# Performance work log

Measured on AMD Instinct MI355X. Metric: run time of the kernel, lower is better.

The kernel has to match this reference:

```python
import jax, jax.numpy as jnp
import numpy as np

B, D_MODEL, N, H = 4, 256, 2048, 4
HEAD_DIM = D_MODEL // H  # 64


def _rotate_half(x):
    # x: [..., d] with d even; pairs (x1, x2) -> (-x2, x1)
    x = x.reshape(x.shape[:-1] + (x.shape[-1] // 2, 2))
    x1, x2 = x[..., 0], x[..., 1]
    return jnp.stack((-x2, x1), axis=-1).reshape(x.shape[:-2] + (-1,))


def _apply_rope(freqs, t):
    # freqs: [2, n, d] (cos, sin); t: [b, h, n, d]
    return t * freqs[0] + _rotate_half(t) * freqs[1]


def setup_inputs() -> dict:
    key = jax.random.key(0)
    ks = jax.random.split(key, 12)
    s = 0.02
    inp = {
        "query": jax.random.normal(ks[0], (B, D_MODEL, N), jnp.float32),
        "key": jax.random.normal(ks[1], (B, D_MODEL, N), jnp.float32),
        "value": jax.random.normal(ks[2], (B, D_MODEL, N), jnp.float32),
        "encoding": jax.random.normal(ks[3], (2, N, HEAD_DIM), jnp.float32),
        "Wq": jax.random.normal(ks[4], (D_MODEL, D_MODEL), jnp.float32) * s,
        "bq": jnp.zeros((D_MODEL,), jnp.float32),
        "Wk": jax.random.normal(ks[5], (D_MODEL, D_MODEL), jnp.float32) * s,
        "bk": jnp.zeros((D_MODEL,), jnp.float32),
        "Wv": jax.random.normal(ks[6], (D_MODEL, D_MODEL), jnp.float32) * s,
        "bv": jnp.zeros((D_MODEL,), jnp.float32),
        "Wm": jax.random.normal(ks[7], (D_MODEL, D_MODEL), jnp.float32) * s,
        "bm": jnp.zeros((D_MODEL,), jnp.float32),
    }
    return inp


def _proj(W, b, x):
    # 1x1 Conv1d == channel matmul: x [b, c_in, n] -> [b, c_out, n]
    return jnp.einsum('oi,bin->bon', W, x) + b[None, :, None]


def reference(query, key, value, encoding, Wq, bq, Wk, bk, Wv, bv, Wm, bm):
    b = query.shape[0]
    # project and split channels into (head_dim, heads): [b, d, h, n]
    q = _proj(Wq, bq, query).reshape(b, HEAD_DIM, H, -1)
    k = _proj(Wk, bk, key).reshape(b, HEAD_DIM, H, -1)
    v = _proj(Wv, bv, value).reshape(b, HEAD_DIM, H, -1)
    # RoPE on [b, h, n, d] layout
    q = jnp.transpose(_apply_rope(encoding, jnp.transpose(q, (0, 2, 3, 1))), (0, 3, 1, 2))
    k = jnp.transpose(_apply_rope(encoding, jnp.transpose(k, (0, 2, 3, 1))), (0, 3, 1, 2))
    # attention: scores [b, h, n, m]
    scores = jnp.einsum('bdhn,bdhm->bhnm', q, k) / jnp.sqrt(jnp.float32(HEAD_DIM))
    prob = jax.nn.softmax(scores, axis=-1)
    x = jnp.einsum('bhnm,bdhm->bdhn', prob, v)
    x = x.reshape(b, HEAD_DIM * H, -1)
    return _proj(Wm, bm, x)
```

## Files before the change

kernel.cpp:

```cpp
#include <hip/hip_runtime.h>
#include <stdint.h>

#define NSEQ 2048

typedef __attribute__((ext_vector_type(4))) float f32x4;
typedef __attribute__((ext_vector_type(8))) short s16x8;
typedef _Float16 f16x8 __attribute__((ext_vector_type(8)));

#define OFF_XT  0u
#define OFF_PO  0u
#define OFF_M   16777216u
#define OFF_L   17301504u
#define OFF_QR  17825792u
#define OFF_KR  22020096u
#define OFF_VT  26214400u

__device__ __forceinline__ short f2h(float f) {
  _Float16 h = (_Float16)f;
  return __builtin_bit_cast(short, h);
}
__device__ __forceinline__ float h2f(short s) {
  return (float)__builtin_bit_cast(_Float16, s);
}
__device__ __forceinline__ int swz128(int row, int slot) {
  return row * 128 + ((slot ^ (row & 7)) << 4);
}
#define MFMA(a, b, c) __builtin_amdgcn_mfma_f32_16x16x32_f16(a, b, c, 0, 0, 0)

__global__ __launch_bounds__(256) void k_trans(const float* __restrict__ q,
    const float* __restrict__ k, const float* __restrict__ v, char* __restrict__ ws) {
  int tensor = blockIdx.z >> 2, b = blockIdx.z & 3;
  const float* src = tensor == 0 ? q : (tensor == 1 ? k : v);
  short* dst = (short*)(ws + OFF_XT) + (tensor * 4 + b) * 524288;
  int n0 = blockIdx.x * 64, i0 = blockIdx.y * 64;
  __shared__ float tile[64][65];
  int t = threadIdx.x;
  int nl = t & 63, ib = (t >> 6) * 16;
#pragma unroll
  for (int r = 0; r < 16; ++r)
    tile[ib + r][nl] = src[(b * 256 + i0 + ib + r) * 2048 + n0 + nl];
  __syncthreads();
  int nr = t >> 2, ic = (t & 3) * 16;
  short tmp[16];
#pragma unroll
  for (int j = 0; j < 16; ++j) tmp[j] = f2h(tile[ic + j][nr]);
  short* dp = &dst[(n0 + nr) * 256 + i0 + ic];
  *(s16x8*)dp = *(const s16x8*)&tmp[0];
  *(s16x8*)(dp + 8) = *(const s16x8*)&tmp[8];
}

__global__ __launch_bounds__(256) void k_proj(const float* __restrict__ Wq,
    const float* __restrict__ Wk, const float* __restrict__ Wv,
    const float* __restrict__ enc, const float* __restrict__ bq,
    const float* __restrict__ bk, const float* __restrict__ bv, char* __restrict__ ws) {
  int proj = blockIdx.z >> 2, b = blockIdx.z & 3;
  const float* W = proj == 0 ? Wq : (proj == 1 ? Wk : Wv);
  const short* X = (const short*)(ws + OFF_XT) + (proj * 4 + b) * 524288;
  int o0 = blockIdx.y * 64, n0 = blockIdx.x * 64;
  __shared__ short As[64 * 64], Bs[64 * 64];
  int t = threadIdx.x, lane = t & 63, g = lane >> 4, c = lane & 15, wave = t >> 6;
  int wr = wave >> 1, wc = wave & 1;
  int row = t >> 2, seg = t & 3;
  f32x4 acc[2][2] = {};
  for (int kk = 0; kk < 4; ++kk) {
    __syncthreads();
    int koff = kk * 64;
    const float* wsrc = &W[(o0 + row) * 256 + koff + seg * 16];
    short ha[16];
#pragma unroll
    for (int q4 = 0; q4 < 4; ++q4) {
      f32x4 wv4 = *(const f32x4*)(wsrc + q4 * 4);
#pragma unroll
      for (int j = 0; j < 4; ++j) ha[q4 * 4 + j] = f2h(wv4[j]);
    }
    *(s16x8*)((char*)As + swz128(row, seg * 2))     = *(const s16x8*)&ha[0];
    *(s16x8*)((char*)As + swz128(row, seg * 2 + 1)) = *(const s16x8*)&ha[8];
    const short* xsrc = &X[(n0 + row) * 256 + koff];
    *(s16x8*)((char*)Bs + swz128(row, seg))     = *(const s16x8*)(xsrc + seg * 8);
    *(s16x8*)((char*)Bs + swz128(row, 4 + seg)) = *(const s16x8*)(xsrc + 32 + seg * 8);
    __syncthreads();
#pragma unroll
    for (int ks = 0; ks < 2; ++ks) {
      f16x8 af[2], bfr[2];
#pragma unroll
      for (int f = 0; f < 2; ++f) {
        af[f]  = *(const f16x8*)((char*)As + swz128(wr * 32 + f * 16 + c, ks * 4 + g));
        bfr[f] = *(const f16x8*)((char*)Bs + swz128(wc * 32 + f * 16 + c, ks * 4 + g));
      }
#pragma unroll
      for (int i = 0; i < 2; ++i)
#pragma unroll
        for (int j = 0; j < 2; ++j)
          acc[i][j] = MFMA(af[i], bfr[j], acc[i][j]);
    }
  }
  const float* bias = proj == 0 ? bq : (proj == 1 ? bk : bv);
  if (proj < 2) {
    short* dst0 = (short*)(ws + (proj == 0 ? OFF_QR : OFF_KR));
    float scale = proj == 0 ? 0.18033688f : 1.0f;
    float sgn = (g & 1) ? 1.0f : -1.0f;
#pragma unroll
    for (int i = 0; i < 2; ++i) {
      int ob = o0 + wr * 32 + i * 16 + g * 4;
      int d = ob >> 2;
#pragma unroll
      for (int j = 0; j < 2; ++j) {
        int n = n0 + wc * 32 + j * 16 + c;
        float cv = enc[n * 64 + d], sv = enc[131072 + n * 64 + d];
#pragma unroll
        for (int r = 0; r < 4; ++r) {
          float val = acc[i][j][r] + bias[ob + r];
          float par = __shfl_xor(val, 16, 64);
          float res = (val * cv + sgn * par * sv) * scale;
          dst0[((b * 4 + r) * 2048 + n) * 64 + d] = f2h(res);
        }
      }
    }
  } else {
    short* dst = (short*)(ws + OFF_VT);
#pragma unroll
    for (int i = 0; i < 2; ++i) {
      int ob = o0 + wr * 32 + i * 16 + g * 4;
      int d = ob >> 2;
#pragma unroll
      for (int j = 0; j < 2; ++j) {
        int n = n0 + wc * 32 + j * 16 + c;
#pragma unroll
        for (int r = 0; r < 4; ++r) {
          float val = acc[i][j][r] + bias[ob + r];
          dst[((b * 4 + r) * 64 + d) * 2048 + n] = f2h(val);
        }
      }
    }
  }
}

__global__ __launch_bounds__(256, 4) void k_attn(char* __restrict__ ws) {
  int bh = blockIdx.y, ms = blockIdx.z;
  int t = threadIdx.x, wave = t >> 6, lane = t & 63, g = lane >> 4, c = lane & 15;
  int nw = blockIdx.x * 64 + wave * 16;
  const short* Q = (const short*)(ws + OFF_QR) + bh * 131072;
  const short* K = (const short*)(ws + OFF_KR) + bh * 131072;
  const short* V = (const short*)(ws + OFF_VT) + bh * 131072;
  __shared__ short Ks[64 * 64], Vs[64 * 64], Ps[4][16 * 64];
  char* Pb = (char*)Ps[wave];
  f16x8 qf0 = *(const f16x8*)&Q[(nw + c) * 64 + g * 8];
  f16x8 qf1 = *(const f16x8*)&Q[(nw + c) * 64 + 32 + g * 8];
  f32x4 po[4] = {};
  float mrun = -1e30f, lrun = 0.f;
  int sr = t >> 3, sl = t & 7;
  const int mb = ms * 512;
  int bsrc = g * 16 + g * 4;

  s16x8 RA[4], RB[4];
  auto LD = [&](int m0, s16x8* R) {
    R[0] = *(const s16x8*)&K[(m0 + sr) * 64 + sl * 8];
    R[1] = *(const s16x8*)&K[(m0 + sr + 32) * 64 + sl * 8];
    R[2] = *(const s16x8*)&V[sr * 2048 + m0 + sl * 8];
    R[3] = *(const s16x8*)&V[(sr + 32) * 2048 + m0 + sl * 8];
  };
  auto ST = [&](const s16x8* R) {
    *(s16x8*)((char*)Ks + swz128(sr, sl))      = R[0];
    *(s16x8*)((char*)Ks + swz128(sr + 32, sl)) = R[1];
    *(s16x8*)((char*)Vs + swz128(sr, sl))      = R[2];
    *(s16x8*)((char*)Vs + swz128(sr + 32, sl)) = R[3];
  };
  auto COMPUTE = [&]() {
    f32x4 s[4] = {};
    __builtin_amdgcn_s_setprio(1);
#pragma unroll
    for (int fj = 0; fj < 4; ++fj) {
      f16x8 k0 = *(const f16x8*)((char*)Ks + swz128(fj * 16 + c, g));
      f16x8 k1 = *(const f16x8*)((char*)Ks + swz128(fj * 16 + c, 4 + g));
      s[fj] = MFMA(k0, qf0, s[fj]);
      s[fj] = MFMA(k1, qf1, s[fj]);
    }
    __builtin_amdgcn_s_setprio(0);
    float t0 = fmaxf(fmaxf(s[0][0], s[0][1]), fmaxf(s[0][2], s[0][3]));
    float t1 = fmaxf(fmaxf(s[1][0], s[1][1]), fmaxf(s[1][2], s[1][3]));
    float t2 = fmaxf(fmaxf(s[2][0], s[2][1]), fmaxf(s[2][2], s[2][3]));
    float t3 = fmaxf(fmaxf(s[3][0], s[3][1]), fmaxf(s[3][2], s[3][3]));
    float rmax = fmaxf(fmaxf(t0, t1), fmaxf(t2, t3));
    rmax = fmaxf(rmax, __shfl_xor(rmax, 16, 64));
    rmax = fmaxf(rmax, __shfl_xor(rmax, 32, 64));
    if (__any(rmax > mrun + 11.5f)) {
      float nm = fmaxf(mrun, rmax);
      float corr = exp2f(mrun - nm);
      mrun = nm;
      lrun *= corr;
#pragma unroll
      for (int r = 0; r < 4; ++r) {
        float corr_r = __shfl(corr, bsrc + r, 64);
#pragma unroll
        for (int fd = 0; fd < 4; ++fd) po[fd][r] *= corr_r;
      }
    }
    float p[4][4], rs = 0.f;
#pragma unroll
    for (int fj = 0; fj < 4; ++fj) {
      f32x4 pv;
#pragma unroll
      for (int r = 0; r < 4; ++r) {
        pv[r] = exp2f(s[fj][r] - mrun);
        p[fj][r] = pv[r];
      }
      rs += (pv[0] + pv[1]) + (pv[2] + pv[3]);
    }
    rs += __shfl_xor(rs, 16, 64);
    rs += __shfl_xor(rs, 32, 64);
    lrun += rs;
#pragma unroll
    for (int fj = 0; fj < 4; ++fj)
#pragma unroll
      for (int r = 0; r < 4; ++r) {
        int mm = fj * 16 + g * 4 + r;
        *(short*)(Pb + swz128(c, mm >> 3) + (mm & 7) * 2) = f2h(p[fj][r]);
      }
    asm volatile("s_waitcnt lgkmcnt(0)" ::: "memory");
    __builtin_amdgcn_sched_barrier(0);
    f16x8 pa0 = *(const f16x8*)(Pb + swz128(c, g));
    f16x8 pa1 = *(const f16x8*)(Pb + swz128(c, 4 + g));
    __builtin_amdgcn_s_setprio(1);
#pragma unroll
    for (int fd = 0; fd < 4; ++fd) {
      int dd = fd * 16 + c;
      f16x8 vb0 = *(const f16x8*)((char*)Vs + swz128(dd, g));
      f16x8 vb1 = *(const f16x8*)((char*)Vs + swz128(dd, 4 + g));
      po[fd] = MFMA(pa0, vb0, po[fd]);
      po[fd] = MFMA(pa1, vb1, po[fd]);
    }
    __builtin_amdgcn_s_setprio(0);
  };

  LD(mb, RA);
  for (int tt = 0; tt < 8; tt += 2) {
    __syncthreads();
    ST(RA);
    LD(mb + (tt + 1) * 64, RB);
    __syncthreads();
    COMPUTE();
    __syncthreads();
    ST(RB);
    if (tt + 2 < 8) LD(mb + (tt + 2) * 64, RA);
    __syncthreads();
    COMPUTE();
  }

  short* PO = (short*)(ws + OFF_PO);
  float* Mm = (float*)(ws + OFF_M);
  float* Ll = (float*)(ws + OFF_L);
  int base = (ms * 16 + bh) * 2048;
  float li[4];
#pragma unroll
  for (int r = 0; r < 4; ++r) li[r] = 1.0f / __shfl(lrun, bsrc + r, 64);
#pragma unroll
  for (int fd = 0; fd < 4; ++fd) {
    int d = fd * 16 + c;
#pragma unroll
    for (int r = 0; r < 4; ++r) {
      int n = nw + g * 4 + r;
      PO[(base + n) * 64 + d] = f2h(po[fd][r] * li[r]);
    }
  }
  if (g == 0) {
    Mm[base + nw + c] = mrun;
    Ll[base + nw + c] = lrun;
  }
}

__global__ __launch_bounds__(256) void k_final(const float* __restrict__ Wm,
    const float* __restrict__ bm, float* __restrict__ out, char* __restrict__ ws) {
  int b = blockIdx.z;
  int o0 = blockIdx.y * 64, n0 = blockIdx.x * 64;
  const short* PO = (const short*)(ws + OFF_PO);
  const float* Mm = (const float*)(ws + OFF_M);
  const float* Ll = (const float*)(ws + OFF_L);
  __shared__ short As[64 * 64], Bs[64 * 64];
  int t = threadIdx.x, lane = t & 63, g = lane >> 4, c = lane & 15, wave = t >> 6;
  int wr = wave >> 1, wc = wave & 1;
  int row = t >> 2, seg = t & 3;
  f32x4 acc[2][2] = {};
  for (int kk = 0; kk < 4; ++kk) {
    __syncthreads();
    short ha[16];
#pragma unroll
    for (int j = 0; j < 16; ++j)
      ha[j] = f2h(Wm[(o0 + row) * 256 + (seg * 16 + j) * 4 + kk]);
    *(s16x8*)((char*)As + swz128(row, seg * 2))     = *(const s16x8*)&ha[0];
    *(s16x8*)((char*)As + swz128(row, seg * 2 + 1)) = *(const s16x8*)&ha[8];
    int bh = b * 4 + kk;
    int nr = n0 + row;
    float m0 = Mm[(0 * 16 + bh) * 2048 + nr], l0 = Ll[(0 * 16 + bh) * 2048 + nr];
    float m1 = Mm[(1 * 16 + bh) * 2048 + nr], l1 = Ll[(1 * 16 + bh) * 2048 + nr];
    float m2 = Mm[(2 * 16 + bh) * 2048 + nr], l2 = Ll[(2 * 16 + bh) * 2048 + nr];
    float m3 = Mm[(3 * 16 + bh) * 2048 + nr], l3 = Ll[(3 * 16 + bh) * 2048 + nr];
    float M = fmaxf(fmaxf(m0, m1), fmaxf(m2, m3));
    float w0 = l0 * exp2f(m0 - M), w1 = l1 * exp2f(m1 - M);
    float w2 = l2 * exp2f(m2 - M), w3 = l3 * exp2f(m3 - M);
    float inv = 1.f / (w0 + w1 + w2 + w3);
    w0 *= inv; w1 *= inv; w2 *= inv; w3 *= inv;
    float cb[16];
    {
      const short* p0 = &PO[((0 * 16 + bh) * 2048 + nr) * 64 + seg * 16];
      const short* p1 = &PO[((1 * 16 + bh) * 2048 + nr) * 64 + seg * 16];
      const short* p2 = &PO[((2 * 16 + bh) * 2048 + nr) * 64 + seg * 16];
      const short* p3 = &PO[((3 * 16 + bh) * 2048 + nr) * 64 + seg * 16];
      s16x8 a0 = *(const s16x8*)p0, a1 = *(const s16x8*)(p0 + 8);
      s16x8 b0 = *(const s16x8*)p1, b1 = *(const s16x8*)(p1 + 8);
      s16x8 c0 = *(const s16x8*)p2, c1 = *(const s16x8*)(p2 + 8);
      s16x8 d0 = *(const s16x8*)p3, d1 = *(const s16x8*)(p3 + 8);
#pragma unroll
      for (int j = 0; j < 8; ++j) {
        cb[j]     = w0 * h2f(a0[j]) + w1 * h2f(b0[j]) + w2 * h2f(c0[j]) + w3 * h2f(d0[j]);
        cb[j + 8] = w0 * h2f(a1[j]) + w1 * h2f(b1[j]) + w2 * h2f(c1[j]) + w3 * h2f(d1[j]);
      }
    }
    short hb[16];
#pragma unroll
    for (int j = 0; j < 16; ++j) hb[j] = f2h(cb[j]);
    *(s16x8*)((char*)Bs + swz128(row, seg * 2))     = *(const s16x8*)&hb[0];
    *(s16x8*)((char*)Bs + swz128(row, seg * 2 + 1)) = *(const s16x8*)&hb[8];
    __syncthreads();
#pragma unroll
    for (int ks = 0; ks < 2; ++ks) {
      f16x8 af[2], bfr[2];
#pragma unroll
      for (int f = 0; f < 2; ++f) {
        af[f]  = *(const f16x8*)((char*)As + swz128(wr * 32 + f * 16 + c, ks * 4 + g));
        bfr[f] = *(const f16x8*)((char*)Bs + swz128(wc * 32 + f * 16 + c, ks * 4 + g));
      }
#pragma unroll
      for (int i = 0; i < 2; ++i)
#pragma unroll
        for (int j = 0; j < 2; ++j)
          acc[i][j] = MFMA(af[i], bfr[j], acc[i][j]);
    }
  }
#pragma unroll
  for (int i = 0; i < 2; ++i) {
    int ob = o0 + wr * 32 + i * 16 + g * 4;
#pragma unroll
    for (int j = 0; j < 2; ++j) {
      int n = n0 + wc * 32 + j * 16 + c;
#pragma unroll
      for (int r = 0; r < 4; ++r)
        out[(b * 256 + ob + r) * 2048 + n] = acc[i][j][r] + bm[ob + r];
    }
  }
}

extern "C" void kernel_launch(void* const* d_in, const int* in_sizes, int n_in,
                              void* d_out, int out_size, void* d_ws, size_t ws_size,
                              hipStream_t stream) {
  (void)in_sizes; (void)n_in; (void)out_size; (void)ws_size;
  const float* q   = (const float*)d_in[0];
  const float* k   = (const float*)d_in[1];
  const float* v   = (const float*)d_in[2];
  const float* enc = (const float*)d_in[3];
  const float* Wq  = (const float*)d_in[4];
  const float* bq  = (const float*)d_in[5];
  const float* Wk  = (const float*)d_in[6];
  const float* bk  = (const float*)d_in[7];
  const float* Wv  = (const float*)d_in[8];
  const float* bv  = (const float*)d_in[9];
  const float* Wm  = (const float*)d_in[10];
  const float* bm  = (const float*)d_in[11];
  char* ws = (char*)d_ws;
  float* out = (float*)d_out;
  hipLaunchKernelGGL(k_trans, dim3(32, 4, 12), dim3(256), 0, stream, q, k, v, ws);
  hipLaunchKernelGGL(k_proj, dim3(32, 4, 12), dim3(256), 0, stream, Wq, Wk, Wv, enc, bq, bk, bv, ws);
  hipLaunchKernelGGL(k_attn, dim3(32, 16, 4), dim3(256), 0, stream, ws);
  hipLaunchKernelGGL(k_final, dim3(32, 4, 4), dim3(256), 0, stream, Wm, bm, out, ws);
}
```

Measured before the change: 161.1 us.

## Process two query tiles per wave in attention and remap blocks across XCDs

Each attention wave now handles 32 query rows (two 16-row MFMA tiles) instead of 16. Each K/V tile loaded into shared memory is reused for twice the work, and the attention grid is halved. Block indices in k_proj, k_attn and k_final are remapped so that neighbouring logical tiles land on the same XCD (blocks are assumed round-robin over 8 XCDs), which should improve L2 locality. The cost is more registers per thread for the doubled accumulators and softmax state, which may reduce occupancy under the 4-blocks-per-CU launch bound.

```diff
diff --git a/kernel.cpp b/kernel.cpp
--- a/kernel.cpp
+++ b/kernel.cpp
@@ -53,10 +53,13 @@
     const float* __restrict__ Wk, const float* __restrict__ Wv,
     const float* __restrict__ enc, const float* __restrict__ bq,
     const float* __restrict__ bk, const float* __restrict__ bv, char* __restrict__ ws) {
-  int proj = blockIdx.z >> 2, b = blockIdx.z & 3;
+  int hid = blockIdx.x + 32 * (blockIdx.y + 4 * blockIdx.z);
+  int fm = (hid & 7) * 192 + (hid >> 3);
+  int yo = fm & 3, xn = (fm >> 2) & 31, z = fm >> 7;
+  int proj = z >> 2, b = z & 3;
   const float* W = proj == 0 ? Wq : (proj == 1 ? Wk : Wv);
   const short* X = (const short*)(ws + OFF_XT) + (proj * 4 + b) * 524288;
-  int o0 = blockIdx.y * 64, n0 = blockIdx.x * 64;
+  int o0 = yo * 64, n0 = xn * 64;
   __shared__ short As[64 * 64], Bs[64 * 64];
   int t = threadIdx.x, lane = t & 63, g = lane >> 4, c = lane & 15, wave = t >> 6;
   int wr = wave >> 1, wc = wave & 1;
@@ -136,18 +139,22 @@
 }
 
 __global__ __launch_bounds__(256, 4) void k_attn(char* __restrict__ ws) {
-  int bh = blockIdx.y, ms = blockIdx.z;
+  int hid = blockIdx.x + 16 * (blockIdx.y + 16 * blockIdx.z);
+  int fm = (hid & 7) * 128 + (hid >> 3);
+  int qx = fm & 15, bh = (fm >> 4) & 15, ms = fm >> 8;
   int t = threadIdx.x, wave = t >> 6, lane = t & 63, g = lane >> 4, c = lane & 15;
-  int nw = blockIdx.x * 64 + wave * 16;
+  int nw = qx * 128 + wave * 32;
   const short* Q = (const short*)(ws + OFF_QR) + bh * 131072;
   const short* K = (const short*)(ws + OFF_KR) + bh * 131072;
   const short* V = (const short*)(ws + OFF_VT) + bh * 131072;
-  __shared__ short Ks[64 * 64], Vs[64 * 64], Ps[4][16 * 64];
+  __shared__ short Ks[64 * 64], Vs[64 * 64], Ps[4][32 * 64];
   char* Pb = (char*)Ps[wave];
-  f16x8 qf0 = *(const f16x8*)&Q[(nw + c) * 64 + g * 8];
-  f16x8 qf1 = *(const f16x8*)&Q[(nw + c) * 64 + 32 + g * 8];
-  f32x4 po[4] = {};
-  float mrun = -1e30f, lrun = 0.f;
+  f16x8 qa0 = *(const f16x8*)&Q[(nw + c) * 64 + g * 8];
+  f16x8 qa1 = *(const f16x8*)&Q[(nw + c) * 64 + 32 + g * 8];
+  f16x8 qb0 = *(const f16x8*)&Q[(nw + 16 + c) * 64 + g * 8];
+  f16x8 qb1 = *(const f16x8*)&Q[(nw + 16 + c) * 64 + 32 + g * 8];
+  f32x4 poA[4] = {}, poB[4] = {};
+  float mrA = -1e30f, lrA = 0.f, mrB = -1e30f, lrB = 0.f;
   int sr = t >> 3, sl = t & 7;
   const int mb = ms * 512;
   int bsrc = g * 16 + g * 4;
@@ -166,68 +173,93 @@
     *(s16x8*)((char*)Vs + swz128(sr + 32, sl)) = R[3];
   };
   auto COMPUTE = [&]() {
-    f32x4 s[4] = {};
+    f32x4 sA[4] = {}, sB[4] = {};
     __builtin_amdgcn_s_setprio(1);
 #pragma unroll
     for (int fj = 0; fj < 4; ++fj) {
       f16x8 k0 = *(const f16x8*)((char*)Ks + swz128(fj * 16 + c, g));
       f16x8 k1 = *(const f16x8*)((char*)Ks + swz128(fj * 16 + c, 4 + g));
-      s[fj] = MFMA(k0, qf0, s[fj]);
-      s[fj] = MFMA(k1, qf1, s[fj]);
+      sA[fj] = MFMA(k0, qa0, sA[fj]);
+      sB[fj] = MFMA(k0, qb0, sB[fj]);
+      sA[fj] = MFMA(k1, qa1, sA[fj]);
+      sB[fj] = MFMA(k1, qb1, sB[fj]);
     }
     __builtin_amdgcn_s_setprio(0);
-    float t0 = fmaxf(fmaxf(s[0][0], s[0][1]), fmaxf(s[0][2], s[0][3]));
-    float t1 = fmaxf(fmaxf(s[1][0], s[1][1]), fmaxf(s[1][2], s[1][3]));
-    float t2 = fmaxf(fmaxf(s[2][0], s[2][1]), fmaxf(s[2][2], s[2][3]));
-    float t3 = fmaxf(fmaxf(s[3][0], s[3][1]), fmaxf(s[3][2], s[3][3]));
-    float rmax = fmaxf(fmaxf(t0, t1), fmaxf(t2, t3));
-    rmax = fmaxf(rmax, __shfl_xor(rmax, 16, 64));
-    rmax = fmaxf(rmax, __shfl_xor(rmax, 32, 64));
-    if (__any(rmax > mrun + 11.5f)) {
-      float nm = fmaxf(mrun, rmax);
-      float corr = exp2f(mrun - nm);
-      mrun = nm;
-      lrun *= corr;
+    float a0 = fmaxf(fmaxf(sA[0][0], sA[0][1]), fmaxf(sA[0][2], sA[0][3]));
+    float a1 = fmaxf(fmaxf(sA[1][0], sA[1][1]), fmaxf(sA[1][2], sA[1][3]));
+    float a2 = fmaxf(fmaxf(sA[2][0], sA[2][1]), fmaxf(sA[2][2], sA[2][3]));
+    float a3 = fmaxf(fmaxf(sA[3][0], sA[3][1]), fmaxf(sA[3][2], sA[3][3]));
+    float b0 = fmaxf(fmaxf(sB[0][0], sB[0][1]), fmaxf(sB[0][2], sB[0][3]));
+    float b1 = fmaxf(fmaxf(sB[1][0], sB[1][1]), fmaxf(sB[1][2], sB[1][3]));
+    float b2 = fmaxf(fmaxf(sB[2][0], sB[2][1]), fmaxf(sB[2][2], sB[2][3]));
+    float b3 = fmaxf(fmaxf(sB[3][0], sB[3][1]), fmaxf(sB[3][2], sB[3][3]));
+    float rmA = fmaxf(fmaxf(a0, a1), fmaxf(a2, a3));
+    float rmB = fmaxf(fmaxf(b0, b1), fmaxf(b2, b3));
+    rmA = fmaxf(rmA, __shfl_xor(rmA, 16, 64));
+    rmB = fmaxf(rmB, __shfl_xor(rmB, 16, 64));
+    rmA = fmaxf(rmA, __shfl_xor(rmA, 32, 64));
+    rmB = fmaxf(rmB, __shfl_xor(rmB, 32, 64));
+    if (__any(rmA > mrA + 11.5f)) {
+      float nm = fmaxf(mrA, rmA);
+      float corr = exp2f(mrA - nm);
+      mrA = nm; lrA *= corr;
 #pragma unroll
       for (int r = 0; r < 4; ++r) {
-        float corr_r = __shfl(corr, bsrc + r, 64);
-#pragma unroll
-        for (int fd = 0; fd < 4; ++fd) po[fd][r] *= corr_r;
-      }
-    }
-    float p[4][4], rs = 0.f;
-#pragma unroll
-    for (int fj = 0; fj < 4; ++fj) {
-      f32x4 pv;
+        float cr = __shfl(corr, bsrc + r, 64);
+#pragma unroll
+        for (int fd = 0; fd < 4; ++fd) poA[fd][r] *= cr;
+      }
+    }
+    if (__any(rmB > mrB + 11.5f)) {
+      float nm = fmaxf(mrB, rmB);
+      float corr = exp2f(mrB - nm);
+      mrB = nm; lrB *= corr;
 #pragma unroll
       for (int r = 0; r < 4; ++r) {
-        pv[r] = exp2f(s[fj][r] - mrun);
-        p[fj][r] = pv[r];
-      }
-      rs += (pv[0] + pv[1]) + (pv[2] + pv[3]);
-    }
-    rs += __shfl_xor(rs, 16, 64);
-    rs += __shfl_xor(rs, 32, 64);
-    lrun += rs;
+        float cr = __shfl(corr, bsrc + r, 64);
+#pragma unroll
+        for (int fd = 0; fd < 4; ++fd) poB[fd][r] *= cr;
+      }
+    }
+    float pA[4][4], pB[4][4], rsA = 0.f, rsB = 0.f;
+#pragma unroll
+    for (int fj = 0; fj < 4; ++fj)
+#pragma unroll
+      for (int r = 0; r < 4; ++r) {
+        pA[fj][r] = exp2f(sA[fj][r] - mrA);
+        pB[fj][r] = exp2f(sB[fj][r] - mrB);
+        rsA += pA[fj][r];
+        rsB += pB[fj][r];
+      }
+    rsA += __shfl_xor(rsA, 16, 64);
+    rsB += __shfl_xor(rsB, 16, 64);
+    rsA += __shfl_xor(rsA, 32, 64);
+    rsB += __shfl_xor(rsB, 32, 64);
+    lrA += rsA; lrB += rsB;
 #pragma unroll
     for (int fj = 0; fj < 4; ++fj)
 #pragma unroll
       for (int r = 0; r < 4; ++r) {
         int mm = fj * 16 + g * 4 + r;
-        *(short*)(Pb + swz128(c, mm >> 3) + (mm & 7) * 2) = f2h(p[fj][r]);
+        *(short*)(Pb + swz128(c, mm >> 3) + (mm & 7) * 2)      = f2h(pA[fj][r]);
+        *(short*)(Pb + swz128(16 + c, mm >> 3) + (mm & 7) * 2) = f2h(pB[fj][r]);
       }
     asm volatile("s_waitcnt lgkmcnt(0)" ::: "memory");
     __builtin_amdgcn_sched_barrier(0);
-    f16x8 pa0 = *(const f16x8*)(Pb + swz128(c, g));
-    f16x8 pa1 = *(const f16x8*)(Pb + swz128(c, 4 + g));
+    f16x8 paA0 = *(const f16x8*)(Pb + swz128(c, g));
+    f16x8 paA1 = *(const f16x8*)(Pb + swz128(c, 4 + g));
+    f16x8 paB0 = *(const f16x8*)(Pb + swz128(16 + c, g));
+    f16x8 paB1 = *(const f16x8*)(Pb + swz128(16 + c, 4 + g));
     __builtin_amdgcn_s_setprio(1);
 #pragma unroll
     for (int fd = 0; fd < 4; ++fd) {
       int dd = fd * 16 + c;
       f16x8 vb0 = *(const f16x8*)((char*)Vs + swz128(dd, g));
       f16x8 vb1 = *(const f16x8*)((char*)Vs + swz128(dd, 4 + g));
-      po[fd] = MFMA(pa0, vb0, po[fd]);
-      po[fd] = MFMA(pa1, vb1, po[fd]);
+      poA[fd] = MFMA(paA0, vb0, poA[fd]);
+      poB[fd] = MFMA(paB0, vb0, poB[fd]);
+      poA[fd] = MFMA(paA1, vb1, poA[fd]);
+      poB[fd] = MFMA(paB1, vb1, poB[fd]);
     }
     __builtin_amdgcn_s_setprio(0);
   };
@@ -250,28 +282,37 @@
   float* Mm = (float*)(ws + OFF_M);
   float* Ll = (float*)(ws + OFF_L);
   int base = (ms * 16 + bh) * 2048;
-  float li[4];
-#pragma unroll
-  for (int r = 0; r < 4; ++r) li[r] = 1.0f / __shfl(lrun, bsrc + r, 64);
+  float liA[4], liB[4];
+#pragma unroll
+  for (int r = 0; r < 4; ++r) {
+    liA[r] = 1.0f / __shfl(lrA, bsrc + r, 64);
+    liB[r] = 1.0f / __shfl(lrB, bsrc + r, 64);
+  }
 #pragma unroll
   for (int fd = 0; fd < 4; ++fd) {
     int d = fd * 16 + c;
 #pragma unroll
     for (int r = 0; r < 4; ++r) {
-      int n = nw + g * 4 + r;
-      PO[(base + n) * 64 + d] = f2h(po[fd][r] * li[r]);
+      int nA = nw + g * 4 + r;
+      int nB = nw + 16 + g * 4 + r;
+      PO[(base + nA) * 64 + d] = f2h(poA[fd][r] * liA[r]);
+      PO[(base + nB) * 64 + d] = f2h(poB[fd][r] * liB[r]);
     }
   }
   if (g == 0) {
-    Mm[base + nw + c] = mrun;
-    Ll[base + nw + c] = lrun;
+    Mm[base + nw + c] = mrA;
+    Ll[base + nw + c] = lrA;
+    Mm[base + nw + 16 + c] = mrB;
+    Ll[base + nw + 16 + c] = lrB;
   }
 }
 
 __global__ __launch_bounds__(256) void k_final(const float* __restrict__ Wm,
     const float* __restrict__ bm, float* __restrict__ out, char* __restrict__ ws) {
-  int b = blockIdx.z;
-  int o0 = blockIdx.y * 64, n0 = blockIdx.x * 64;
+  int hid = blockIdx.x + 32 * (blockIdx.y + 4 * blockIdx.z);
+  int fm = (hid & 7) * 64 + (hid >> 3);
+  int yo = fm & 3, xn = (fm >> 2) & 31, b = fm >> 7;
+  int o0 = yo * 64, n0 = xn * 64;
   const short* PO = (const short*)(ws + OFF_PO);
   const float* Mm = (const float*)(ws + OFF_M);
   const float* Ll = (const float*)(ws + OFF_L);
@@ -369,6 +410,6 @@
   float* out = (float*)d_out;
   hipLaunchKernelGGL(k_trans, dim3(32, 4, 12), dim3(256), 0, stream, q, k, v, ws);
   hipLaunchKernelGGL(k_proj, dim3(32, 4, 12), dim3(256), 0, stream, Wq, Wk, Wv, enc, bq, bk, bv, ws);
-  hipLaunchKernelGGL(k_attn, dim3(32, 16, 4), dim3(256), 0, stream, ws);
+  hipLaunchKernelGGL(k_attn, dim3(16, 16, 4), dim3(256), 0, stream, ws);
   hipLaunchKernelGGL(k_final, dim3(32, 4, 4), dim3(256), 0, stream, Wm, bm, out, ws);
 }
```

Result: slower. 177.2 us (+10.0%).
